# Kernel tuning notes

Hardware: AMD Instinct MI355X
Metric: run time of the kernel (lower is better)

Reference implementation:

```python
import jax, jax.numpy as jnp
import numpy as np
import math

B, S, D, H = 4, 1024, 512, 8
HD = D // H
HID = 4 * D


def clinear(xr, xi, lm, ph, bm=None, bp=None):
    # magnitude-phase parameterized complex linear: W = exp(lm) * e^{i*ph}
    mag = jnp.exp(lm)
    wr = mag * jnp.cos(ph)
    wi = mag * jnp.sin(ph)
    r = xr @ wr.T - xi @ wi.T
    i = xr @ wi.T + xi @ wr.T
    if bm is not None:
        r = r + bm * jnp.cos(bp)
        i = i + bm * jnp.sin(bp)
    return r, i


def cln(xr, xi, gr, gi, br, bi, eps=1e-6):
    mr = xr.mean(-1, keepdims=True)
    mi = xi.mean(-1, keepdims=True)
    cr, ci = xr - mr, xi - mi
    var = (cr * cr + ci * ci).mean(-1, keepdims=True)
    inv = 1.0 / jnp.sqrt(var + eps)
    nr, ni = cr * inv, ci * inv
    return nr * gr - ni * gi + br, nr * gi + ni * gr + bi


def rotate_half(x):
    h = x.shape[-1] // 2
    return jnp.concatenate([-x[..., h:], x[..., :h]], axis=-1)


def split_heads(x):  # (B,S,D) -> (B,H,S,HD)
    return x.reshape(B, S, H, HD).transpose(0, 2, 1, 3)


def merge_heads(x):  # (B,H,S,HD) -> (B,S,D)
    return x.transpose(0, 2, 1, 3).reshape(B, S, D)


def setup_inputs() -> dict:
    key = jax.random.key(0)
    ks = iter(jax.random.split(key, 64))

    def lin(o_f, i_f):
        lm = jax.random.normal(next(ks), (o_f, i_f)) * 0.1 - 0.5 * math.log(i_f)
        ph = jax.random.uniform(next(ks), (o_f, i_f), minval=-math.pi, maxval=math.pi)
        return lm.astype(jnp.float32), ph.astype(jnp.float32)

    inp = {}
    inp['x_real'] = jax.random.normal(next(ks), (B, S, D), dtype=jnp.float32)
    inp['x_imag'] = jax.random.normal(next(ks), (B, S, D), dtype=jnp.float32)
    inp['ln1_gr'] = jnp.ones(D); inp['ln1_gi'] = jnp.zeros(D)
    inp['ln1_br'] = jnp.zeros(D); inp['ln1_bi'] = jnp.zeros(D)
    for nm in ['q', 'k', 'v', 'o']:
        lm, ph = lin(D, D)
        inp[nm + '_lm'] = lm; inp[nm + '_ph'] = ph
        inp[nm + '_bm'] = jnp.zeros(D); inp[nm + '_bp'] = jnp.zeros(D)
    inp['ln2_gr'] = jnp.ones(D); inp['ln2_gi'] = jnp.zeros(D)
    inp['ln2_br'] = jnp.zeros(D); inp['ln2_bi'] = jnp.zeros(D)
    inp['gate_lm'], inp['gate_ph'] = lin(HID, D)
    inp['up_lm'], inp['up_ph'] = lin(HID, D)
    inp['down_lm'], inp['down_ph'] = lin(D, HID)
    return inp


def reference(x_real, x_imag, ln1_gr, ln1_gi, ln1_br, ln1_bi,
              q_lm, q_ph, q_bm, q_bp, k_lm, k_ph, k_bm, k_bp,
              v_lm, v_ph, v_bm, v_bp, o_lm, o_ph, o_bm, o_bp,
              ln2_gr, ln2_gi, ln2_br, ln2_bi,
              gate_lm, gate_ph, up_lm, up_ph, down_lm, down_ph):
    # --- pre-attention complex LayerNorm ---
    hr, hi = cln(x_real, x_imag, ln1_gr, ln1_gi, ln1_br, ln1_bi)

    # --- complex QKV projections ---
    qr, qi = clinear(hr, hi, q_lm, q_ph, q_bm, q_bp)
    kr, ki = clinear(hr, hi, k_lm, k_ph, k_bm, k_bp)
    vr, vi = clinear(hr, hi, v_lm, v_ph, v_bm, v_bp)
    qr, qi = split_heads(qr), split_heads(qi)
    kr, ki = split_heads(kr), split_heads(ki)
    vr, vi = split_heads(vr), split_heads(vi)

    # --- complex RoPE (same real rotation applied to real & imag parts) ---
    pos = jnp.arange(S, dtype=jnp.float32)
    inv_freq = 1.0 / (10000.0 ** (jnp.arange(0, HD, 2, dtype=jnp.float32) / HD))
    freqs = pos[:, None] * inv_freq[None, :]          # (S, HD/2)
    cos = jnp.concatenate([jnp.cos(freqs)] * 2, -1)[None, None]  # (1,1,S,HD)
    sin = jnp.concatenate([jnp.sin(freqs)] * 2, -1)[None, None]
    rot = lambda x: x * cos + rotate_half(x) * sin
    qr, qi, kr, ki = rot(qr), rot(qi), rot(kr), rot(ki)

    # --- Hermitian attention: Re(q . conj(k)) = qr.kr + qi.ki ---
    scale = 1.0 / math.sqrt(HD)
    scores = (jnp.einsum('bhqd,bhkd->bhqk', qr, kr)
              + jnp.einsum('bhqd,bhkd->bhqk', qi, ki)) * scale
    causal = jnp.tril(jnp.ones((S, S), dtype=bool))
    scores = jnp.where(causal, scores, jnp.float32(-1e9))
    attn = jax.nn.softmax(scores, axis=-1)            # real-valued weights
    ar = jnp.einsum('bhqk,bhkd->bhqd', attn, vr)
    ai = jnp.einsum('bhqk,bhkd->bhqd', attn, vi)
    ar, ai = merge_heads(ar), merge_heads(ai)
    ar, ai = clinear(ar, ai, o_lm, o_ph, o_bm, o_bp)

    # --- residual + LN2 ---
    res_r, res_i = x_real + ar, x_imag + ai
    hr, hi = cln(res_r, res_i, ln2_gr, ln2_gi, ln2_br, ln2_bi)

    # --- complex gated FFN (SwiGLU-style, complex gating) ---
    gr_, gi_ = clinear(hr, hi, gate_lm, gate_ph)
    s = jax.nn.sigmoid(jnp.sqrt(gr_ * gr_ + gi_ * gi_))  # sigmoid(|gate|)
    gar, gai = gr_ * s, gi_ * s
    ur, ui = clinear(hr, hi, up_lm, up_ph)
    hid_r = gar * ur - gai * ui
    hid_i = gar * ui + gai * ur
    dr, di = clinear(hid_r, hid_i, down_lm, down_ph)

    out_r = res_r + dr
    out_i = res_i + di
    return jnp.stack([out_r, out_i], axis=0)  # (2, B, S, D)
```

## Files before the change

### kernel.cpp

```cpp
#include <hip/hip_runtime.h>
#include <math.h>

#define kB 4
#define kS 1024
#define kD 512
#define kH 8
#define kHD 64
#define kHID 2048
#define kNT (kB * kS)
#define kBSD (kNT * kD)

typedef __attribute__((ext_vector_type(8))) short bf16x8;
typedef __attribute__((ext_vector_type(4))) float f32x4;

#define AS1 __attribute__((address_space(1)))
#define AS3 __attribute__((address_space(3)))

__device__ __forceinline__ float bf2f(unsigned short u) {
  return __uint_as_float(((unsigned int)u) << 16);
}
__device__ __forceinline__ unsigned short f2bf(float f) {
  unsigned int u = __float_as_uint(f);
  u += 0x7fffu + ((u >> 16) & 1u);
  return (unsigned short)(u >> 16);
}

__global__ __launch_bounds__(256) void build_wA_kernel(
    const float* __restrict__ qlm, const float* __restrict__ qph,
    const float* __restrict__ klm, const float* __restrict__ kph,
    const float* __restrict__ vlm, const float* __restrict__ vph,
    const float* __restrict__ olm, const float* __restrict__ oph,
    const float* __restrict__ qbm, const float* __restrict__ qbp,
    const float* __restrict__ kbm, const float* __restrict__ kbp,
    const float* __restrict__ vbm, const float* __restrict__ vbp,
    const float* __restrict__ obm, const float* __restrict__ obp,
    unsigned short* __restrict__ Wqkv, unsigned short* __restrict__ Wo,
    float* __restrict__ qkvBias, float* __restrict__ oBias) {
  int bx = blockIdx.x;
  if (bx >= 4096) {
    int gid = (bx - 4096) * 256 + threadIdx.x;
    int seg = gid >> 9, m = gid & 511;
    const float* bm = seg == 0 ? qbm : seg == 1 ? kbm : seg == 2 ? vbm : obm;
    const float* bp = seg == 0 ? qbp : seg == 1 ? kbp : seg == 2 ? vbp : obp;
    float s, c;
    __sincosf(bp[m], &s, &c);
    float br = bm[m] * c, bi = bm[m] * s;
    if (seg < 3) {
      int h = m >> 6, d = m & 63;
      qkvBias[seg * 1024 + h * 128 + d] = br;
      qkvBias[seg * 1024 + h * 128 + 64 + d] = bi;
    } else {
      oBias[m] = br;
      oBias[512 + m] = bi;
    }
    return;
  }
  int gid = bx * 256 + threadIdx.x;
  int seg = gid >> 18;
  int id = gid & 262143;
  const float* lm = seg == 0 ? qlm : seg == 1 ? klm : seg == 2 ? vlm : olm;
  const float* ph = seg == 0 ? qph : seg == 1 ? kph : seg == 2 ? vph : oph;
  float mm = __expf(lm[id]);
  float s, c;
  __sincosf(ph[id], &s, &c);
  float wr = mm * c, wi = mm * s;
  int m = id >> 9, k = id & 511;
  if (seg < 3) {
    int h = m >> 6, d = m & 63;
    size_t rowR = (size_t)seg * 1024 + h * 128 + d;
    size_t rowI = rowR + 64;
    Wqkv[rowR * 1024 + k] = f2bf(wr);
    Wqkv[rowR * 1024 + 512 + k] = f2bf(-wi);
    Wqkv[rowI * 1024 + k] = f2bf(wi);
    Wqkv[rowI * 1024 + 512 + k] = f2bf(wr);
  } else {
    Wo[(size_t)m * 1024 + k] = f2bf(wr);
    Wo[(size_t)m * 1024 + 512 + k] = f2bf(-wi);
    Wo[(size_t)(512 + m) * 1024 + k] = f2bf(wi);
    Wo[(size_t)(512 + m) * 1024 + 512 + k] = f2bf(wr);
  }
}

__global__ __launch_bounds__(256) void build_wB_kernel(
    const float* __restrict__ glm, const float* __restrict__ gph,
    const float* __restrict__ ulm, const float* __restrict__ uph,
    const float* __restrict__ dlm, const float* __restrict__ dph,
    unsigned short* __restrict__ Wgu, unsigned short* __restrict__ Wd) {
  int gid = blockIdx.x * 256 + threadIdx.x;
  int seg = gid >> 20;
  int id = gid & 1048575;
  const float* lm = seg == 0 ? glm : seg == 1 ? ulm : dlm;
  const float* ph = seg == 0 ? gph : seg == 1 ? uph : dph;
  float mm = __expf(lm[id]);
  float s, c;
  __sincosf(ph[id], &s, &c);
  float wr = mm * c, wi = mm * s;
  if (seg < 2) {
    int T = id >> 9, k = id & 511;
    size_t base = (size_t)(T >> 4) * 64 + (T & 15);
    size_t rR = base + (seg * 2 + 0) * 16;
    size_t rI = base + (seg * 2 + 1) * 16;
    Wgu[rR * 1024 + k] = f2bf(wr);
    Wgu[rR * 1024 + 512 + k] = f2bf(-wi);
    Wgu[rI * 1024 + k] = f2bf(wi);
    Wgu[rI * 1024 + 512 + k] = f2bf(wr);
  } else {
    int m = id >> 11, j = id & 2047;
    Wd[(size_t)m * 4096 + 2 * j] = f2bf(wr);
    Wd[(size_t)m * 4096 + 2 * j + 1] = f2bf(-wi);
    Wd[(size_t)(512 + m) * 4096 + 2 * j] = f2bf(wi);
    Wd[(size_t)(512 + m) * 4096 + 2 * j + 1] = f2bf(wr);
  }
}

__global__ __launch_bounds__(256) void cln_kernel(
    const float* __restrict__ xr, const float* __restrict__ xi, int stride,
    const float* __restrict__ g_r, const float* __restrict__ g_i,
    const float* __restrict__ b_r, const float* __restrict__ b_i,
    unsigned short* __restrict__ out) {
  int w = threadIdx.x >> 6, lane = threadIdx.x & 63;
  int t = blockIdx.x * 4 + w;
  int d0 = lane * 8;
  const float* xrt = xr + (size_t)t * stride + d0;
  const float* xit = xi + (size_t)t * stride + d0;
  float4 a0 = *(const float4*)&xrt[0];
  float4 a1 = *(const float4*)&xrt[4];
  float4 c0 = *(const float4*)&xit[0];
  float4 c1 = *(const float4*)&xit[4];

  float s1 = a0.x + a0.y + a0.z + a0.w + a1.x + a1.y + a1.z + a1.w;
  float s2 = c0.x + c0.y + c0.z + c0.w + c1.x + c1.y + c1.z + c1.w;
#pragma unroll
  for (int off = 1; off < 64; off <<= 1) {
    s1 += __shfl_xor(s1, off);
    s2 += __shfl_xor(s2, off);
  }
  float mr = s1 * (1.f / kD), mi = s2 * (1.f / kD);

  float ar[8] = {a0.x, a0.y, a0.z, a0.w, a1.x, a1.y, a1.z, a1.w};
  float ai[8] = {c0.x, c0.y, c0.z, c0.w, c1.x, c1.y, c1.z, c1.w};
  float v = 0.f;
#pragma unroll
  for (int e = 0; e < 8; e++) {
    float cr = ar[e] - mr, ci = ai[e] - mi;
    v += cr * cr + ci * ci;
  }
#pragma unroll
  for (int off = 1; off < 64; off <<= 1) v += __shfl_xor(v, off);
  float inv = rsqrtf(v * (1.f / kD) + 1e-6f);

  float4 g0 = *(const float4*)&g_r[d0];
  float4 g1 = *(const float4*)&g_r[d0 + 4];
  float4 h0 = *(const float4*)&g_i[d0];
  float4 h1 = *(const float4*)&g_i[d0 + 4];
  float4 p0 = *(const float4*)&b_r[d0];
  float4 p1 = *(const float4*)&b_r[d0 + 4];
  float4 q0 = *(const float4*)&b_i[d0];
  float4 q1 = *(const float4*)&b_i[d0 + 4];
  float gr[8] = {g0.x, g0.y, g0.z, g0.w, g1.x, g1.y, g1.z, g1.w};
  float gi[8] = {h0.x, h0.y, h0.z, h0.w, h1.x, h1.y, h1.z, h1.w};
  float br[8] = {p0.x, p0.y, p0.z, p0.w, p1.x, p1.y, p1.z, p1.w};
  float bi[8] = {q0.x, q0.y, q0.z, q0.w, q1.x, q1.y, q1.z, q1.w};

  unsigned short pr[8], pi[8];
#pragma unroll
  for (int e = 0; e < 8; e++) {
    float nr = (ar[e] - mr) * inv;
    float ni = (ai[e] - mi) * inv;
    pr[e] = f2bf(nr * gr[e] - ni * gi[e] + br[e]);
    pi[e] = f2bf(nr * gi[e] + ni * gr[e] + bi[e]);
  }
  unsigned short* ot = out + (size_t)t * 1024 + d0;
  *(bf16x8*)&ot[0] = *(const bf16x8*)pr;
  *(bf16x8*)&ot[512] = *(const bf16x8*)pi;
}

__global__ __launch_bounds__(256) void cgemm_mfma_kernel(
    const unsigned short* __restrict__ X, int ldx,
    const unsigned short* __restrict__ Wt, int K,
    const float* __restrict__ bias, int mode,
    unsigned short* __restrict__ outb, int ldo,
    unsigned short* __restrict__ vtb) {
  __shared__ unsigned short Sh[128 * 64 * 2];
  unsigned short* Xs = Sh;
  unsigned short* Ws = Sh + 8192;

  const int tid = threadIdx.x;
  const int w = tid >> 6;
  const int lane = tid & 63;
  const int quad = lane >> 4;
  const int l15 = lane & 15;
  const int m0 = blockIdx.x * 128;
  const int n0 = blockIdx.y * 128;
  const int wm = (w & 1) * 64;
  const int wn = (w >> 1) * 64;

  const int rsub = lane >> 3;
  const int grow = w * 32 + rsub;
  const int gcol = ((lane & 7) ^ rsub) * 8;
  const unsigned short* gx = X + (size_t)(n0 + grow) * ldx + gcol;
  const unsigned short* gw = Wt + (size_t)(m0 + grow) * K + gcol;

  const int rg = (l15 & 7);

  f32x4 acc[4][4];
#pragma unroll
  for (int i = 0; i < 4; i++)
#pragma unroll
    for (int j = 0; j < 4; j++) acc[i][j] = (f32x4){0.f, 0.f, 0.f, 0.f};

  for (int k0 = 0; k0 < K; k0 += 64) {
    __syncthreads();
#pragma unroll
    for (int t = 0; t < 4; t++) {
      __builtin_amdgcn_global_load_lds((const AS1 void*)(gx + (size_t)t * 8 * ldx + k0),
                                       (AS3 void*)&Xs[w * 2048 + t * 512], 16, 0, 0);
      __builtin_amdgcn_global_load_lds((const AS1 void*)(gw + (size_t)t * 8 * K + k0),
                                       (AS3 void*)&Ws[w * 2048 + t * 512], 16, 0, 0);
    }
    __syncthreads();

#pragma unroll
    for (int ks = 0; ks < 2; ks++) {
      const int gsel = ((ks * 4 + quad) ^ rg) * 8;
      bf16x8 af[4], bf[4];
#pragma unroll
      for (int t = 0; t < 4; t++) {
        af[t] = *(const bf16x8*)&Xs[(wn + t * 16 + l15) * 64 + gsel];
        bf[t] = *(const bf16x8*)&Ws[(wm + t * 16 + l15) * 64 + gsel];
      }
#pragma unroll
      for (int i = 0; i < 4; i++)
#pragma unroll
        for (int j = 0; j < 4; j++)
          acc[i][j] = __builtin_amdgcn_mfma_f32_16x16x32_bf16(af[i], bf[j], acc[i][j], 0, 0, 0);
    }
  }

  if (mode == 4) {
    int T = ((m0 + wm) >> 6) * 16 + l15;
#pragma unroll
    for (int i = 0; i < 4; ++i) {
      int row0 = n0 + wn + i * 16 + quad * 4;
#pragma unroll
      for (int r = 0; r < 4; ++r) {
        float gr = acc[i][0][r], gi = acc[i][1][r];
        float ur = acc[i][2][r], ui = acc[i][3][r];
        float sg = __builtin_amdgcn_rcpf(1.f + __expf(-sqrtf(gr * gr + gi * gi)));
        float gar = gr * sg, gai = gi * sg;
        unsigned int pk = (unsigned)f2bf(gar * ur - gai * ui)
                        | ((unsigned)f2bf(gar * ui + gai * ur) << 16);
        *(unsigned int*)&outb[(size_t)(row0 + r) * ldo + 2 * T] = pk;
      }
    }
  } else if (mode == 3 && m0 < 2048) {
#pragma unroll
    for (int j = 0; j < 4; ++j) {
      float bv = bias[m0 + wm + j * 16 + l15];
#pragma unroll
      for (int i = 0; i < 4; ++i)
#pragma unroll
        for (int r = 0; r < 4; ++r) acc[i][j][r] += bv;
    }
    const int sbase = ((n0 + wn) & (kS - 1)) + quad * 4;
#pragma unroll
    for (int j01 = 0; j01 < 2; ++j01) {
      float fi = (float)(j01 * 16 + l15);
      float f = __expf(fi * -0.28782313662425572f);
      float c1, s1, c16, s16, cI, sI;
      __sincosf(f, &s1, &c1);
      __sincosf(16.f * f, &s16, &c16);
      __sincosf((float)sbase * f, &sI, &cI);
#pragma unroll
      for (int i = 0; i < 4; ++i) {
        float cc = cI, ss = sI;
#pragma unroll
        for (int r = 0; r < 4; ++r) {
          float x0 = acc[i][j01][r], x1 = acc[i][j01 + 2][r];
          acc[i][j01][r] = x0 * cc - x1 * ss;
          acc[i][j01 + 2][r] = x1 * cc + x0 * ss;
          float cn = cc * c1 - ss * s1;
          ss = ss * c1 + cc * s1;
          cc = cn;
        }
        float cn = cI * c16 - sI * s16;
        sI = sI * c16 + cI * s16;
        cI = cn;
      }
    }
#pragma unroll
    for (int j = 0; j < 4; ++j) {
      int col = m0 + wm + j * 16 + l15;
#pragma unroll
      for (int i = 0; i < 4; ++i) {
        int row0 = n0 + wn + i * 16 + quad * 4;
#pragma unroll
        for (int r = 0; r < 4; ++r)
          outb[(size_t)(row0 + r) * ldo + col] = f2bf(acc[i][j][r]);
      }
    }
  } else {
    unsigned short* Ts = Sh;
#pragma unroll
    for (int p = 0; p < 2; ++p) {
      __syncthreads();
      if ((w & 1) == p) {
#pragma unroll
        for (int j = 0; j < 4; ++j) {
          float bv = bias[m0 + wm + j * 16 + l15];
          int fl = j * 16 + l15;
#pragma unroll
          for (int i = 0; i < 4; ++i) {
            int tk = wn + i * 16 + quad * 4;
#pragma unroll
            for (int r = 0; r < 4; ++r)
              Ts[fl * 130 + tk + r] = f2bf(acc[i][j][r] + bv);
          }
        }
      }
      __syncthreads();
      {
        int fr = tid >> 2, seg = tid & 3;
        int f = (m0 - 2048) + p * 64 + fr;
        int hh = f >> 7, dc = f & 127;
        int bb = n0 >> 10, sbase2 = (n0 & (kS - 1)) + seg * 32;
        unsigned short* dst = &vtb[(size_t)((bb * 8 + hh) * 128 + dc) * 1024 + sbase2];
        const unsigned short* src = &Ts[fr * 130 + seg * 32];
#pragma unroll
        for (int u = 0; u < 4; u++)
          *(bf16x8*)(dst + u * 8) = *(const bf16x8*)(src + u * 8);
      }
    }
  }
}

__global__ __launch_bounds__(256) void cgemm_mfma_n64_kernel(
    const unsigned short* __restrict__ X, int ldx,
    const unsigned short* __restrict__ Wt, int K,
    const float* __restrict__ bias, int mode,
    const float* __restrict__ resr, const float* __restrict__ resi,
    float* __restrict__ outf) {
  __shared__ unsigned short Xs[64 * 64];
  __shared__ unsigned short Ws[128 * 64];

  const int tid = threadIdx.x;
  const int w = tid >> 6;
  const int lane = tid & 63;
  const int quad = lane >> 4;
  const int l15 = lane & 15;
  const int m0 = blockIdx.x * 128;
  const int n0 = blockIdx.y * 64;
  const int wm = (w & 1) * 64;
  const int wn = (w >> 1) * 32;

  const int rsub = lane >> 3;
  const int gcol = ((lane & 7) ^ rsub) * 8;
  const unsigned short* gx = X + (size_t)(n0 + w * 16 + rsub) * ldx + gcol;
  const unsigned short* gw = Wt + (size_t)(m0 + w * 32 + rsub) * K + gcol;
  const int rg = (l15 & 7);

  f32x4 acc[2][4];
#pragma unroll
  for (int i = 0; i < 2; i++)
#pragma unroll
    for (int j = 0; j < 4; j++) acc[i][j] = (f32x4){0.f, 0.f, 0.f, 0.f};

  for (int k0 = 0; k0 < K; k0 += 64) {
    __syncthreads();
#pragma unroll
    for (int t = 0; t < 2; t++)
      __builtin_amdgcn_global_load_lds((const AS1 void*)(gx + (size_t)t * 8 * ldx + k0),
                                       (AS3 void*)&Xs[w * 1024 + t * 512], 16, 0, 0);
#pragma unroll
    for (int t = 0; t < 4; t++)
      __builtin_amdgcn_global_load_lds((const AS1 void*)(gw + (size_t)t * 8 * K + k0),
                                       (AS3 void*)&Ws[w * 2048 + t * 512], 16, 0, 0);
    __syncthreads();

#pragma unroll
    for (int ks = 0; ks < 2; ks++) {
      const int gsel = ((ks * 4 + quad) ^ rg) * 8;
      bf16x8 af[2], bf[4];
#pragma unroll
      for (int t = 0; t < 2; t++)
        af[t] = *(const bf16x8*)&Xs[(wn + t * 16 + l15) * 64 + gsel];
#pragma unroll
      for (int t = 0; t < 4; t++)
        bf[t] = *(const bf16x8*)&Ws[(wm + t * 16 + l15) * 64 + gsel];
#pragma unroll
      for (int i = 0; i < 2; i++)
#pragma unroll
        for (int j = 0; j < 4; j++)
          acc[i][j] = __builtin_amdgcn_mfma_f32_16x16x32_bf16(af[i], bf[j], acc[i][j], 0, 0, 0);
    }
  }

#pragma unroll
  for (int j = 0; j < 4; ++j) {
    int col = m0 + wm + j * 16 + l15;
    float bv = bias ? bias[col] : 0.f;
#pragma unroll
    for (int i = 0; i < 2; ++i) {
      int row0 = n0 + wn + i * 16 + quad * 4;
#pragma unroll
      for (int r = 0; r < 4; ++r) {
        int row = row0 + r;
        float val = acc[i][j][r] + bv;
        if (mode == 1) {
          float xres = (col < 512) ? resr[(size_t)row * 512 + col]
                                   : resi[(size_t)row * 512 + col - 512];
          outf[(size_t)row * 1024 + col] = val + xres;
        } else {
          float rv = resr[(size_t)row * 1024 + col] + val;
          size_t dd = (col < 512) ? ((size_t)row * 512 + col)
                                  : ((size_t)kBSD + (size_t)row * 512 + (col - 512));
          outf[dd] = rv;
        }
      }
    }
  }
}

__global__ __launch_bounds__(256) void attn_mfma_kernel(
    const unsigned short* __restrict__ qkv,
    const unsigned short* __restrict__ vt,
    unsigned short* __restrict__ out) {
  __shared__ unsigned short Ks[64 * 136];
  __shared__ unsigned short Vs[128 * 72];
  __shared__ unsigned short Ps[4 * 16 * 72];

  const int tid = threadIdx.x;
  const int w = tid >> 6;
  const int lane = tid & 63;
  const int quad = lane >> 4;
  const int l15 = lane & 15;

  int bid = blockIdx.x;
  int qt = bid & 15;
  if ((bid >> 4) & 1) qt = 15 - qt;
  const int h = (bid >> 4) & 7;
  const int b = bid >> 7;
  const int q0 = qt * 64;
  const int wrow0 = q0 + w * 16;

  bf16x8 qa[4];
  {
    size_t base = (size_t)(b * kS + wrow0 + l15) * 3072 + h * 128;
#pragma unroll
    for (int ks = 0; ks < 4; ks++)
      qa[ks] = *(const bf16x8*)&qkv[base + ks * 32 + quad * 8];
  }

  f32x4 oacc[8];
#pragma unroll
  for (int dt = 0; dt < 8; dt++) oacc[dt] = (f32x4){0.f, 0.f, 0.f, 0.f};
  float m_r[4] = {-1e30f, -1e30f, -1e30f, -1e30f};
  float l_r[4] = {0.f, 0.f, 0.f, 0.f};

  const int nkt = qt + 1;
  const float cexp = 0.1803368801f;

  const unsigned short* gkbase = qkv + 1024 + h * 128;
  const unsigned short* gvbase = vt + (size_t)((b * 8 + h) * 128) * 1024;

  for (int kt = 0; kt < nkt; ++kt) {
    const int k0 = kt * 64;
    __syncthreads();
    {
      const unsigned short* gk = gkbase + (size_t)(b * kS + k0) * 3072;
      int ch = tid * 4;
#pragma unroll
      for (int u = 0; u < 4; u++) {
        int r = (ch + u) >> 4, cc = ((ch + u) & 15) * 8;
        *(bf16x8*)&Ks[r * 136 + cc] = *(const bf16x8*)&gk[(size_t)r * 3072 + cc];
      }
#pragma unroll
      for (int u = 0; u < 4; u++) {
        int vr = (ch + u) >> 3, vc = ((ch + u) & 7) * 8;
        *(bf16x8*)&Vs[vr * 72 + vc] = *(const bf16x8*)&gvbase[(size_t)vr * 1024 + k0 + vc];
      }
    }
    __syncthreads();

    f32x4 s[4];
#pragma unroll
    for (int ns = 0; ns < 4; ns++) {
      s[ns] = (f32x4){0.f, 0.f, 0.f, 0.f};
#pragma unroll
      for (int ks = 0; ks < 4; ks++) {
        bf16x8 kb = *(const bf16x8*)&Ks[(ns * 16 + l15) * 136 + ks * 32 + quad * 8];
        s[ns] = __builtin_amdgcn_mfma_f32_16x16x32_bf16(qa[ks], kb, s[ns], 0, 0, 0);
      }
    }

    if (k0 + 63 > wrow0) {
#pragma unroll
      for (int r = 0; r < 4; r++) {
        int qrow = wrow0 + quad * 4 + r;
#pragma unroll
        for (int ns = 0; ns < 4; ns++)
          if (k0 + ns * 16 + l15 > qrow) s[ns][r] = -1e30f;
      }
    }

    float alpha[4];
#pragma unroll
    for (int r = 0; r < 4; r++) {
      float mx = fmaxf(fmaxf(s[0][r], s[1][r]), fmaxf(s[2][r], s[3][r]));
      mx = fmaxf(mx, __shfl_xor(mx, 1));
      mx = fmaxf(mx, __shfl_xor(mx, 2));
      mx = fmaxf(mx, __shfl_xor(mx, 4));
      mx = fmaxf(mx, __shfl_xor(mx, 8));
      float mn = fmaxf(m_r[r], mx);
      float al = exp2f((m_r[r] - mn) * cexp);
      m_r[r] = mn;
      float rs = 0.f;
#pragma unroll
      for (int ns = 0; ns < 4; ns++) {
        float p = exp2f((s[ns][r] - mn) * cexp);
        s[ns][r] = p;
        rs += p;
      }
      rs += __shfl_xor(rs, 1);
      rs += __shfl_xor(rs, 2);
      rs += __shfl_xor(rs, 4);
      rs += __shfl_xor(rs, 8);
      l_r[r] = l_r[r] * al + rs;
      alpha[r] = al;
    }

#pragma unroll
    for (int dt = 0; dt < 8; dt++)
#pragma unroll
      for (int r = 0; r < 4; r++) oacc[dt][r] *= alpha[r];

    unsigned short* pw = &Ps[w * 1152];
#pragma unroll
    for (int r = 0; r < 4; r++) {
      int q = quad * 4 + r;
#pragma unroll
      for (int ns = 0; ns < 4; ns++)
        pw[q * 72 + ns * 16 + l15] = f2bf(s[ns][r]);
    }
    bf16x8 pa0 = *(const bf16x8*)&pw[l15 * 72 + quad * 8];
    bf16x8 pa1 = *(const bf16x8*)&pw[l15 * 72 + 32 + quad * 8];

#pragma unroll
    for (int dt = 0; dt < 8; dt++) {
      bf16x8 vb0 = *(const bf16x8*)&Vs[(dt * 16 + l15) * 72 + quad * 8];
      bf16x8 vb1 = *(const bf16x8*)&Vs[(dt * 16 + l15) * 72 + 32 + quad * 8];
      oacc[dt] = __builtin_amdgcn_mfma_f32_16x16x32_bf16(pa0, vb0, oacc[dt], 0, 0, 0);
      oacc[dt] = __builtin_amdgcn_mfma_f32_16x16x32_bf16(pa1, vb1, oacc[dt], 0, 0, 0);
    }
  }

  float inv[4];
#pragma unroll
  for (int r = 0; r < 4; r++) inv[r] = __builtin_amdgcn_rcpf(l_r[r]);
#pragma unroll
  for (int dt = 0; dt < 8; dt++) {
    int dcat = dt * 16 + l15;
    int col = (dcat < 64) ? (h * 64 + dcat) : (512 + h * 64 + dcat - 64);
#pragma unroll
    for (int r = 0; r < 4; r++) {
      int tok = b * kS + wrow0 + quad * 4 + r;
      out[(size_t)tok * 1024 + col] = f2bf(oacc[dt][r] * inv[r]);
    }
  }
}

extern "C" void kernel_launch(void* const* d_in, const int* in_sizes, int n_in,
                              void* d_out, int out_size, void* d_ws, size_t ws_size,
                              hipStream_t stream) {
  const float* x_real = (const float*)d_in[0];
  const float* x_imag = (const float*)d_in[1];
  const float* ln1_gr = (const float*)d_in[2];
  const float* ln1_gi = (const float*)d_in[3];
  const float* ln1_br = (const float*)d_in[4];
  const float* ln1_bi = (const float*)d_in[5];
  const float* q_lm = (const float*)d_in[6];
  const float* q_ph = (const float*)d_in[7];
  const float* q_bm = (const float*)d_in[8];
  const float* q_bp = (const float*)d_in[9];
  const float* k_lm = (const float*)d_in[10];
  const float* k_ph = (const float*)d_in[11];
  const float* k_bm = (const float*)d_in[12];
  const float* k_bp = (const float*)d_in[13];
  const float* v_lm = (const float*)d_in[14];
  const float* v_ph = (const float*)d_in[15];
  const float* v_bm = (const float*)d_in[16];
  const float* v_bp = (const float*)d_in[17];
  const float* o_lm = (const float*)d_in[18];
  const float* o_ph = (const float*)d_in[19];
  const float* o_bm = (const float*)d_in[20];
  const float* o_bp = (const float*)d_in[21];
  const float* ln2_gr = (const float*)d_in[22];
  const float* ln2_gi = (const float*)d_in[23];
  const float* ln2_br = (const float*)d_in[24];
  const float* ln2_bi = (const float*)d_in[25];
  const float* gate_lm = (const float*)d_in[26];
  const float* gate_ph = (const float*)d_in[27];
  const float* up_lm = (const float*)d_in[28];
  const float* up_ph = (const float*)d_in[29];
  const float* down_lm = (const float*)d_in[30];
  const float* down_ph = (const float*)d_in[31];

  char* wsb = (char*)d_ws;
  unsigned short* Wqkv = (unsigned short*)(wsb + 0);
  unsigned short* Wo   = (unsigned short*)(wsb + 6291456);
  unsigned short* Wgu  = (unsigned short*)(wsb + 8388608);
  unsigned short* Wd   = (unsigned short*)(wsb + 25165824);
  float* qkvBias = (float*)(wsb + 33554432);
  float* oBias   = (float*)(wsb + 33566720);
  float* res     = (float*)(wsb + 33570816);
  unsigned short* H = (unsigned short*)(wsb + 50348032);
  char* big = wsb + 58736640;
  unsigned short* qkv     = (unsigned short*)big;
  unsigned short* attnout = (unsigned short*)(big + 25165824);
  unsigned short* vtb     = (unsigned short*)(big + 33554432);
  unsigned short* hid     = (unsigned short*)big;

  float* outf = (float*)d_out;

  build_wA_kernel<<<4104, 256, 0, stream>>>(q_lm, q_ph, k_lm, k_ph, v_lm, v_ph,
                                            o_lm, o_ph, q_bm, q_bp, k_bm, k_bp,
                                            v_bm, v_bp, o_bm, o_bp,
                                            Wqkv, Wo, qkvBias, oBias);
  build_wB_kernel<<<12288, 256, 0, stream>>>(gate_lm, gate_ph, up_lm, up_ph,
                                             down_lm, down_ph, Wgu, Wd);

  cln_kernel<<<kNT / 4, 256, 0, stream>>>(x_real, x_imag, 512, ln1_gr, ln1_gi, ln1_br, ln1_bi, H);

  {
    dim3 g(3072 / 128, kNT / 128);
    cgemm_mfma_kernel<<<g, 256, 0, stream>>>(H, 1024, Wqkv, 1024, qkvBias, 3, qkv, 3072, vtb);
  }

  attn_mfma_kernel<<<kB * kH * (kS / 64), 256, 0, stream>>>(qkv, vtb, attnout);

  {
    dim3 g(1024 / 128, kNT / 64);
    cgemm_mfma_n64_kernel<<<g, 256, 0, stream>>>(attnout, 1024, Wo, 1024, oBias, 1,
                                                 x_real, x_imag, res);
  }

  cln_kernel<<<kNT / 4, 256, 0, stream>>>(res, res + 512, 1024, ln2_gr, ln2_gi, ln2_br, ln2_bi, H);

  {
    dim3 g(8192 / 128, kNT / 128);
    cgemm_mfma_kernel<<<g, 256, 0, stream>>>(H, 1024, Wgu, 1024, nullptr, 4, hid, 4096, nullptr);
  }

  {
    dim3 g(1024 / 128, kNT / 64);
    cgemm_mfma_n64_kernel<<<g, 256, 0, stream>>>(hid, 4096, Wd, 4096, nullptr, 2,
                                                 res, nullptr, outf);
  }
}
```

Before: 433.5 us.

## Fuse LN1 into weight build, vectorize FFN weight build, deepen out-proj K tile

Folds the first complex LayerNorm into the build_wA launch as extra blocks, removing one kernel launch. It also makes build_wB process two elements per thread with packed 32/64-bit stores, and doubles the K step of the n64 output-projection GEMM to 128 with a new XOR swizzle. The attention block-to-(batch, head, q-tile) mapping is reordered, and the LN kernels now read gamma/beta per element instead of as float4 vectors. The larger GEMM tile doubles LDS use and halves the number of barriers.

```diff
diff --git a/kernel.cpp b/kernel.cpp
--- a/kernel.cpp
+++ b/kernel.cpp
@@ -23,6 +23,9 @@
   unsigned int u = __float_as_uint(f);
   u += 0x7fffu + ((u >> 16) & 1u);
   return (unsigned short)(u >> 16);
+}
+__device__ __forceinline__ unsigned int pack2(unsigned short a, unsigned short b) {
+  return (unsigned)a | ((unsigned)b << 16);
 }
 
 __global__ __launch_bounds__(256) void build_wA_kernel(
@@ -34,9 +37,55 @@
     const float* __restrict__ kbm, const float* __restrict__ kbp,
     const float* __restrict__ vbm, const float* __restrict__ vbp,
     const float* __restrict__ obm, const float* __restrict__ obp,
+    const float* __restrict__ xr, const float* __restrict__ xi,
+    const float* __restrict__ g_r, const float* __restrict__ g_i,
+    const float* __restrict__ b_r, const float* __restrict__ b_i,
     unsigned short* __restrict__ Wqkv, unsigned short* __restrict__ Wo,
-    float* __restrict__ qkvBias, float* __restrict__ oBias) {
+    float* __restrict__ qkvBias, float* __restrict__ oBias,
+    unsigned short* __restrict__ H) {
   int bx = blockIdx.x;
+  if (bx >= 4104) {
+    int w = threadIdx.x >> 6, lane = threadIdx.x & 63;
+    int t = (bx - 4104) * 4 + w;
+    int d0 = lane * 8;
+    const float* xrt = xr + (size_t)t * 512 + d0;
+    const float* xit = xi + (size_t)t * 512 + d0;
+    float4 a0 = *(const float4*)&xrt[0];
+    float4 a1 = *(const float4*)&xrt[4];
+    float4 c0 = *(const float4*)&xit[0];
+    float4 c1 = *(const float4*)&xit[4];
+    float s1 = a0.x + a0.y + a0.z + a0.w + a1.x + a1.y + a1.z + a1.w;
+    float s2 = c0.x + c0.y + c0.z + c0.w + c1.x + c1.y + c1.z + c1.w;
+#pragma unroll
+    for (int off = 1; off < 64; off <<= 1) {
+      s1 += __shfl_xor(s1, off);
+      s2 += __shfl_xor(s2, off);
+    }
+    float mr = s1 * (1.f / kD), mi = s2 * (1.f / kD);
+    float ar[8] = {a0.x, a0.y, a0.z, a0.w, a1.x, a1.y, a1.z, a1.w};
+    float ai[8] = {c0.x, c0.y, c0.z, c0.w, c1.x, c1.y, c1.z, c1.w};
+    float v = 0.f;
+#pragma unroll
+    for (int e = 0; e < 8; e++) {
+      float cr = ar[e] - mr, ci = ai[e] - mi;
+      v += cr * cr + ci * ci;
+    }
+#pragma unroll
+    for (int off = 1; off < 64; off <<= 1) v += __shfl_xor(v, off);
+    float inv = rsqrtf(v * (1.f / kD) + 1e-6f);
+    unsigned short pr[8], pi[8];
+#pragma unroll
+    for (int e = 0; e < 8; e++) {
+      float nr = (ar[e] - mr) * inv;
+      float ni = (ai[e] - mi) * inv;
+      pr[e] = f2bf(nr * g_r[d0 + e] - ni * g_i[d0 + e] + b_r[d0 + e]);
+      pi[e] = f2bf(nr * g_i[d0 + e] + ni * g_r[d0 + e] + b_i[d0 + e]);
+    }
+    unsigned short* ot = H + (size_t)t * 1024 + d0;
+    *(bf16x8*)&ot[0] = *(const bf16x8*)pr;
+    *(bf16x8*)&ot[512] = *(const bf16x8*)pi;
+    return;
+  }
   if (bx >= 4096) {
     int gid = (bx - 4096) * 256 + threadIdx.x;
     int seg = gid >> 9, m = gid & 511;
@@ -87,29 +136,35 @@
     const float* __restrict__ dlm, const float* __restrict__ dph,
     unsigned short* __restrict__ Wgu, unsigned short* __restrict__ Wd) {
   int gid = blockIdx.x * 256 + threadIdx.x;
-  int seg = gid >> 20;
-  int id = gid & 1048575;
+  int seg = gid >> 19;
+  int id0 = (gid & 524287) * 2;
   const float* lm = seg == 0 ? glm : seg == 1 ? ulm : dlm;
   const float* ph = seg == 0 ? gph : seg == 1 ? uph : dph;
-  float mm = __expf(lm[id]);
-  float s, c;
-  __sincosf(ph[id], &s, &c);
-  float wr = mm * c, wi = mm * s;
+  float2 lm2 = *(const float2*)&lm[id0];
+  float2 ph2 = *(const float2*)&ph[id0];
+  float m0 = __expf(lm2.x), m1 = __expf(lm2.y);
+  float s0, c0, s1, c1;
+  __sincosf(ph2.x, &s0, &c0);
+  __sincosf(ph2.y, &s1, &c1);
+  float wr0 = m0 * c0, wi0 = m0 * s0;
+  float wr1 = m1 * c1, wi1 = m1 * s1;
   if (seg < 2) {
-    int T = id >> 9, k = id & 511;
+    int T = id0 >> 9, k = id0 & 511;
     size_t base = (size_t)(T >> 4) * 64 + (T & 15);
     size_t rR = base + (seg * 2 + 0) * 16;
     size_t rI = base + (seg * 2 + 1) * 16;
-    Wgu[rR * 1024 + k] = f2bf(wr);
-    Wgu[rR * 1024 + 512 + k] = f2bf(-wi);
-    Wgu[rI * 1024 + k] = f2bf(wi);
-    Wgu[rI * 1024 + 512 + k] = f2bf(wr);
+    *(unsigned int*)&Wgu[rR * 1024 + k] = pack2(f2bf(wr0), f2bf(wr1));
+    *(unsigned int*)&Wgu[rR * 1024 + 512 + k] = pack2(f2bf(-wi0), f2bf(-wi1));
+    *(unsigned int*)&Wgu[rI * 1024 + k] = pack2(f2bf(wi0), f2bf(wi1));
+    *(unsigned int*)&Wgu[rI * 1024 + 512 + k] = pack2(f2bf(wr0), f2bf(wr1));
   } else {
-    int m = id >> 11, j = id & 2047;
-    Wd[(size_t)m * 4096 + 2 * j] = f2bf(wr);
-    Wd[(size_t)m * 4096 + 2 * j + 1] = f2bf(-wi);
-    Wd[(size_t)(512 + m) * 4096 + 2 * j] = f2bf(wi);
-    Wd[(size_t)(512 + m) * 4096 + 2 * j + 1] = f2bf(wr);
+    int m = id0 >> 11, j = id0 & 2047;
+    ushort4 a;
+    a.x = f2bf(wr0); a.y = f2bf(-wi0); a.z = f2bf(wr1); a.w = f2bf(-wi1);
+    *(ushort4*)&Wd[(size_t)m * 4096 + 2 * j] = a;
+    ushort4 b;
+    b.x = f2bf(wi0); b.y = f2bf(wr0); b.z = f2bf(wi1); b.w = f2bf(wr1);
+    *(ushort4*)&Wd[(size_t)(512 + m) * 4096 + 2 * j] = b;
   }
 }
 
@@ -149,26 +204,13 @@
   for (int off = 1; off < 64; off <<= 1) v += __shfl_xor(v, off);
   float inv = rsqrtf(v * (1.f / kD) + 1e-6f);
 
-  float4 g0 = *(const float4*)&g_r[d0];
-  float4 g1 = *(const float4*)&g_r[d0 + 4];
-  float4 h0 = *(const float4*)&g_i[d0];
-  float4 h1 = *(const float4*)&g_i[d0 + 4];
-  float4 p0 = *(const float4*)&b_r[d0];
-  float4 p1 = *(const float4*)&b_r[d0 + 4];
-  float4 q0 = *(const float4*)&b_i[d0];
-  float4 q1 = *(const float4*)&b_i[d0 + 4];
-  float gr[8] = {g0.x, g0.y, g0.z, g0.w, g1.x, g1.y, g1.z, g1.w};
-  float gi[8] = {h0.x, h0.y, h0.z, h0.w, h1.x, h1.y, h1.z, h1.w};
-  float br[8] = {p0.x, p0.y, p0.z, p0.w, p1.x, p1.y, p1.z, p1.w};
-  float bi[8] = {q0.x, q0.y, q0.z, q0.w, q1.x, q1.y, q1.z, q1.w};
-
   unsigned short pr[8], pi[8];
 #pragma unroll
   for (int e = 0; e < 8; e++) {
     float nr = (ar[e] - mr) * inv;
     float ni = (ai[e] - mi) * inv;
-    pr[e] = f2bf(nr * gr[e] - ni * gi[e] + br[e]);
-    pi[e] = f2bf(nr * gi[e] + ni * gr[e] + bi[e]);
+    pr[e] = f2bf(nr * g_r[d0 + e] - ni * g_i[d0 + e] + b_r[d0 + e]);
+    pi[e] = f2bf(nr * g_i[d0 + e] + ni * g_r[d0 + e] + b_i[d0 + e]);
   }
   unsigned short* ot = out + (size_t)t * 1024 + d0;
   *(bf16x8*)&ot[0] = *(const bf16x8*)pr;
@@ -248,8 +290,7 @@
         float ur = acc[i][2][r], ui = acc[i][3][r];
         float sg = __builtin_amdgcn_rcpf(1.f + __expf(-sqrtf(gr * gr + gi * gi)));
         float gar = gr * sg, gai = gi * sg;
-        unsigned int pk = (unsigned)f2bf(gar * ur - gai * ui)
-                        | ((unsigned)f2bf(gar * ui + gai * ur) << 16);
+        unsigned int pk = pack2(f2bf(gar * ur - gai * ui), f2bf(gar * ui + gai * ur));
         *(unsigned int*)&outb[(size_t)(row0 + r) * ldo + 2 * T] = pk;
       }
     }
@@ -340,8 +381,8 @@
     const float* __restrict__ bias, int mode,
     const float* __restrict__ resr, const float* __restrict__ resi,
     float* __restrict__ outf) {
-  __shared__ unsigned short Xs[64 * 64];
-  __shared__ unsigned short Ws[128 * 64];
+  __shared__ unsigned short Xs[64 * 128];
+  __shared__ unsigned short Ws[128 * 128];
 
   const int tid = threadIdx.x;
   const int w = tid >> 6;
@@ -353,40 +394,42 @@
   const int wm = (w & 1) * 64;
   const int wn = (w >> 1) * 32;
 
-  const int rsub = lane >> 3;
-  const int gcol = ((lane & 7) ^ rsub) * 8;
-  const unsigned short* gx = X + (size_t)(n0 + w * 16 + rsub) * ldx + gcol;
-  const unsigned short* gw = Wt + (size_t)(m0 + w * 32 + rsub) * K + gcol;
-  const int rg = (l15 & 7);
-
   f32x4 acc[2][4];
 #pragma unroll
   for (int i = 0; i < 2; i++)
 #pragma unroll
     for (int j = 0; j < 4; j++) acc[i][j] = (f32x4){0.f, 0.f, 0.f, 0.f};
 
-  for (int k0 = 0; k0 < K; k0 += 64) {
+  for (int k0 = 0; k0 < K; k0 += 128) {
     __syncthreads();
 #pragma unroll
-    for (int t = 0; t < 2; t++)
-      __builtin_amdgcn_global_load_lds((const AS1 void*)(gx + (size_t)t * 8 * ldx + k0),
-                                       (AS3 void*)&Xs[w * 1024 + t * 512], 16, 0, 0);
-#pragma unroll
-    for (int t = 0; t < 4; t++)
-      __builtin_amdgcn_global_load_lds((const AS1 void*)(gw + (size_t)t * 8 * K + k0),
-                                       (AS3 void*)&Ws[w * 2048 + t * 512], 16, 0, 0);
+    for (int t = 0; t < 4; t++) {
+      int key = t * 4 + quad;
+      int gc = (l15 ^ key) * 8;
+      __builtin_amdgcn_global_load_lds(
+          (const AS1 void*)(X + (size_t)(n0 + w * 16 + t * 4 + quad) * ldx + k0 + gc),
+          (AS3 void*)&Xs[w * 2048 + t * 512], 16, 0, 0);
+    }
+#pragma unroll
+    for (int t = 0; t < 8; t++) {
+      int key = (t * 4 + quad) & 15;
+      int gc = (l15 ^ key) * 8;
+      __builtin_amdgcn_global_load_lds(
+          (const AS1 void*)(Wt + (size_t)(m0 + w * 32 + t * 4 + quad) * K + k0 + gc),
+          (AS3 void*)&Ws[w * 4096 + t * 512], 16, 0, 0);
+    }
     __syncthreads();
 
 #pragma unroll
-    for (int ks = 0; ks < 2; ks++) {
-      const int gsel = ((ks * 4 + quad) ^ rg) * 8;
+    for (int ks = 0; ks < 4; ks++) {
+      const int gsel = ((ks * 4 + quad) ^ l15) * 8;
       bf16x8 af[2], bf[4];
 #pragma unroll
       for (int t = 0; t < 2; t++)
-        af[t] = *(const bf16x8*)&Xs[(wn + t * 16 + l15) * 64 + gsel];
+        af[t] = *(const bf16x8*)&Xs[(wn + t * 16 + l15) * 128 + gsel];
 #pragma unroll
       for (int t = 0; t < 4; t++)
-        bf[t] = *(const bf16x8*)&Ws[(wm + t * 16 + l15) * 64 + gsel];
+        bf[t] = *(const bf16x8*)&Ws[(wm + t * 16 + l15) * 128 + gsel];
 #pragma unroll
       for (int i = 0; i < 2; i++)
 #pragma unroll
@@ -436,10 +479,12 @@
   const int l15 = lane & 15;
 
   int bid = blockIdx.x;
-  int qt = bid & 15;
-  if ((bid >> 4) & 1) qt = 15 - qt;
-  const int h = (bid >> 4) & 7;
-  const int b = bid >> 7;
+  int second = bid >> 8;
+  int u = bid & 255;
+  int t_ = u & 15;
+  const int qt = second ? (15 - t_) : t_;
+  const int h = (u >> 4) & 7;
+  const int b = second * 2 + (u >> 7);
   const int q0 = qt * 64;
   const int wrow0 = q0 + w * 16;
 
@@ -470,13 +515,13 @@
       const unsigned short* gk = gkbase + (size_t)(b * kS + k0) * 3072;
       int ch = tid * 4;
 #pragma unroll
-      for (int u = 0; u < 4; u++) {
-        int r = (ch + u) >> 4, cc = ((ch + u) & 15) * 8;
+      for (int u2 = 0; u2 < 4; u2++) {
+        int r = (ch + u2) >> 4, cc = ((ch + u2) & 15) * 8;
         *(bf16x8*)&Ks[r * 136 + cc] = *(const bf16x8*)&gk[(size_t)r * 3072 + cc];
       }
 #pragma unroll
-      for (int u = 0; u < 4; u++) {
-        int vr = (ch + u) >> 3, vc = ((ch + u) & 7) * 8;
+      for (int u2 = 0; u2 < 4; u2++) {
+        int vr = (ch + u2) >> 3, vc = ((ch + u2) & 7) * 8;
         *(bf16x8*)&Vs[vr * 72 + vc] = *(const bf16x8*)&gvbase[(size_t)vr * 1024 + k0 + vc];
       }
     }
@@ -622,14 +667,14 @@
 
   float* outf = (float*)d_out;
 
-  build_wA_kernel<<<4104, 256, 0, stream>>>(q_lm, q_ph, k_lm, k_ph, v_lm, v_ph,
+  build_wA_kernel<<<5128, 256, 0, stream>>>(q_lm, q_ph, k_lm, k_ph, v_lm, v_ph,
                                             o_lm, o_ph, q_bm, q_bp, k_bm, k_bp,
                                             v_bm, v_bp, o_bm, o_bp,
-                                            Wqkv, Wo, qkvBias, oBias);
-  build_wB_kernel<<<12288, 256, 0, stream>>>(gate_lm, gate_ph, up_lm, up_ph,
-                                             down_lm, down_ph, Wgu, Wd);
-
-  cln_kernel<<<kNT / 4, 256, 0, stream>>>(x_real, x_imag, 512, ln1_gr, ln1_gi, ln1_br, ln1_bi, H);
+                                            x_real, x_imag, ln1_gr, ln1_gi,
+                                            ln1_br, ln1_bi,
+                                            Wqkv, Wo, qkvBias, oBias, H);
+  build_wB_kernel<<<6144, 256, 0, stream>>>(gate_lm, gate_ph, up_lm, up_ph,
+                                            down_lm, down_ph, Wgu, Wd);
 
   {
     dim3 g(3072 / 128, kNT / 128);
```

Measured after the change: 408.9 us. 5.7% less time.
